# Kernel tuning notes

Measured on AMD Instinct MI355X. Metric: run time of the kernel, lower is better.

## Reference

```python
import jax, jax.numpy as jnp
import numpy as np
from jax import lax

BS, K, N = 8, 8, 16            # batch, gathers per sample, picks per curve
T, WG = 3072, 64               # gather time samples, traces
H, WC = 256, 256               # CVEncoder ScaleSize
RH, RW = 1024, 512             # resize (also GatherEncoder outLen=RH)
T0, T1 = 0.0, 7000.0           # tInt[0], tInt[-1]


def setup_inputs() -> dict:
    key = jax.random.key(0)
    ks = jax.random.split(key, 8)
    gather = jax.random.normal(ks[0], (BS, K, T, WG), jnp.float32)
    # cv: times sorted, strictly > 0, within [T0, T1]; velocities within VMM range
    times = jnp.sort(jax.random.uniform(ks[1], (BS, K, N), minval=100.0, maxval=T1), axis=-1)
    vels = jnp.sort(jax.random.uniform(ks[2], (BS, K, N), minval=1500.0, maxval=4500.0), axis=-1)
    cv = jnp.stack([times, vels], axis=-1).astype(jnp.float32)
    VMM = jnp.tile(jnp.array([1500.0, 4500.0], jnp.float32), (BS, 1))
    def cw(k, shape):
        return (jax.random.normal(k, shape, jnp.float32) * 0.1)
    params = dict(
        w1=cw(ks[3], (1, 1, 3, 3)), b1=jnp.zeros((1,), jnp.float32), g1=jnp.ones((1,), jnp.float32), be1=jnp.zeros((1,), jnp.float32),
        w2=cw(ks[4], (2, 3, 3, 3)), b2=jnp.zeros((2,), jnp.float32), g2=jnp.ones((2,), jnp.float32), be2=jnp.zeros((2,), jnp.float32),
        w3=cw(ks[5], (1, 2, 3, 2)), b3=jnp.zeros((1,), jnp.float32), g3=jnp.ones((1,), jnp.float32), be3=jnp.zeros((1,), jnp.float32),
        wf=cw(ks[6], (1, 1, 3, 3)), bf=jnp.zeros((1,), jnp.float32), gf=jnp.ones((1,), jnp.float32), bef=jnp.zeros((1,), jnp.float32),
    )
    return {"gather": gather, "cv": cv, "VMM": VMM, **params}


def _conv(x, w, b, stride, pad):
    y = lax.conv_general_dilated(x, w, stride, pad, dimension_numbers=("NCHW", "OIHW", "NCHW"))
    return y + b[None, :, None, None]


def _bn(x, g, b, eps=1e-5):
    # training-mode BatchNorm2d: stats over (N, H, W)
    m = jnp.mean(x, (0, 2, 3), keepdims=True)
    v = jnp.var(x, (0, 2, 3), keepdims=True)
    return (x - m) / jnp.sqrt(v + eps) * g[None, :, None, None] + b[None, :, None, None]


def _lrelu(x):
    return jnp.where(x >= 0, x, 0.1 * x)


def _cbl(x, w, b, g, be, stride):
    return _lrelu(_bn(_conv(x, w, b, stride, "VALID"), g, be))


def _maxpool(x, k):
    p = k // 2
    return lax.reduce_window(x, -jnp.inf, lax.max, (1, 1, k, k), (1, 1, 1, 1),
                             ((0, 0), (0, 0), (p, p), (p, p)))


def _cv_mask(cv, VMM):
    # normalize times to fractional row index and velocities to fractional col index
    dt = (T1 - T0) / (H - 1)
    t_idx = (cv[..., 0] - T0) / dt                                        # (BS,K,N)
    dv = (VMM[:, 1] - VMM[:, 0]) / (WC - 1)                               # (BS,)
    v_idx = (cv[..., 1] - VMM[:, 0, None, None]) / dv[:, None, None]      # (BS,K,N)
    t_flat = t_idx.reshape(-1, N)
    v_flat = v_idx.reshape(-1, N)
    tq = jnp.arange(H, dtype=jnp.float32)
    # per-curve piecewise-linear interpolation of v over the time grid
    v_curve = jax.vmap(lambda xp, fp: jnp.interp(tq, xp, fp))(t_flat, v_flat)  # (M,H)
    v_int = jnp.clip(v_curve.astype(jnp.int32), 0, WC - 1)
    M = BS * K
    mask = jnp.full((M, H, WC), 0.01, jnp.float32)
    mask = mask.at[jnp.arange(M)[:, None], jnp.arange(H)[None, :], v_int].add(0.9)
    mask = mask.reshape(BS, K, H, WC)
    # bilinear resize, half-pixel centers == torch align_corners=False
    return jax.image.resize(mask, (BS, K, RH, RW), method="linear")


def _forward(gather, cv, VMM, w1, b1, g1, be1, w2, b2, g2, be2, w3, b3, g3, be3, wf, bf, gf, bef):
    cv_mask = lax.stop_gradient(_cv_mask(cv, VMM))          # CVEncoder runs under no_grad
    x = gather.reshape(-1, 1, T, WG)                        # (BS*K,1,T,WG)
    x = x / jnp.max(jnp.abs(x))                             # mode='mute': keep sign
    x = _cbl(x, w1, b1, g1, be1, (3, 2))                    # (M,1,1024,31)
    xcat = jnp.concatenate([x, _maxpool(x, 3), _maxpool(x, 5)], axis=1)
    x = _cbl(xcat, w2, b2, g2, be2, (3, 2))                 # (M,2,341,15)
    x = _cbl(x, w3, b3, g3, be3, (3, 2))                    # (M,1,113,7)
    x = jax.image.resize(x, (x.shape[0], 1, RH, 1), method="linear")
    genr = x.reshape(BS, K, RH, 1)
    mix = jnp.sum(genr * cv_mask, axis=1, keepdims=True)    # (BS,1,RH,RW)
    y = _conv(mix, wf, bf, (1, 1), ((1, 1), (1, 1)))
    return _lrelu(_bn(y, gf, bef))


def reference(gather, cv, VMM, w1, b1, g1, be1, w2, b2, g2, be2, w3, b3, g3, be3, wf, bf, gf, bef):
    return _forward(gather, cv, VMM, w1, b1, g1, be1, w2, b2, g2, be2, w3, b3, g3, be3, wf, bf, gf, bef)
```

## Files before the change

kernel.cpp:

```cpp
#include <hip/hip_runtime.h>
#include <math.h>

#define BSZ 8
#define KG  8
#define NP  16
#define MM  64
#define TT  3072
#define WGN 64
#define HH  256
#define WCN 256
#define RHN 1024
#define RWN 512

#define C1H 1024
#define C1W 31
#define C2H 341
#define C2W 15
#define C3H 113
#define C3W 7

#define N1 (MM*C1H*C1W)
#define N2 (MM*C2H*C2W)
#define N3 (MM*C3H*C3W)
#define NF (BSZ*RHN*RWN)

#define SL 8

#define OFF_VINT 768
#define OFF_Y1   (OFF_VINT + MM*HH*4)
#define OFF_Y2   (OFF_Y1  + N1*4)
#define OFF_Y3   (OFF_Y2  + 2*N2*4)
#define OFF_GENR (OFF_Y3  + N3*4)

__device__ __forceinline__ void blockAdd2(double s, double ss, double* o0, double* o1) {
    __shared__ double red[4][2];
    __syncthreads();
    int lane = threadIdx.x & 63, wid = threadIdx.x >> 6;
#pragma unroll
    for (int off = 32; off > 0; off >>= 1) {
        s  += __shfl_down(s,  off, 64);
        ss += __shfl_down(ss, off, 64);
    }
    if (lane == 0) { red[wid][0] = s; red[wid][1] = ss; }
    __syncthreads();
    if (threadIdx.x == 0) {
        double a = 0, b = 0;
        int nw = blockDim.x >> 6;
        for (int i = 0; i < nw; i++) { a += red[i][0]; b += red[i][1]; }
        int slot = blockIdx.x & (SL - 1);
        atomicAdd(&o0[slot], a); atomicAdd(&o1[slot], b);
    }
}

__device__ __forceinline__ float2 bn_ab(const double* __restrict__ sums, int c,
                                        const float* __restrict__ g,
                                        const float* __restrict__ be, double n) {
    double sum = 0, sumsq = 0;
#pragma unroll
    for (int j = 0; j < SL; j++) {
        sum   += sums[(2 * c) * SL + j];
        sumsq += sums[(2 * c + 1) * SL + j];
    }
    double mean = sum / n;
    double var  = sumsq / n - mean * mean;
    double a = (double)g[c] / sqrt(var + 1e-5);
    return make_float2((float)a, (float)((double)be[c] - mean * a));
}

__global__ void k_conv1(const float* __restrict__ g, const float* __restrict__ w1,
                        const float* __restrict__ b1,
                        float* __restrict__ y1, double* sums) {
    float w[9];
#pragma unroll
    for (int i = 0; i < 9; i++) w[i] = w1[i];
    float bb = b1[0];
    double s = 0, ss = 0;
    int stride = gridDim.x * blockDim.x;
    for (int idx = blockIdx.x * blockDim.x + threadIdx.x; idx < N1; idx += stride) {
        int ow = idx % C1W;
        int t2 = idx / C1W;
        int oh = t2 % C1H;
        int m  = t2 / C1H;
        const float* xp = g + (size_t)m * TT * WGN + (size_t)(oh * 3) * WGN + ow * 2;
        float acc = bb;
#pragma unroll
        for (int r = 0; r < 3; r++)
#pragma unroll
            for (int c = 0; c < 3; c++) acc += w[r * 3 + c] * xp[r * WGN + c];
        y1[idx] = acc;
        s += acc; ss += (double)acc * (double)acc;
    }
    blockAdd2(s, ss, &sums[0], &sums[SL]);
}

#define F2_OH 32
#define F2_NCH 11
#define F2_NRMAX (3*F2_OH + 4)
__global__ void k_fused2(const float* __restrict__ y1, const double* __restrict__ sums_r,
                         const float* __restrict__ g1, const float* __restrict__ be1,
                         const float* __restrict__ w2, const float* __restrict__ b2,
                         float* __restrict__ y2, double* sums) {
    __shared__ float sact[F2_NRMAX][32];
    __shared__ float sr3[F2_NRMAX][32];
    __shared__ float sr5[F2_NRMAX][32];
    float2 ab1 = bn_ab(sums_r, 0, g1, be1, (double)N1);
    int m   = blockIdx.x / F2_NCH;
    int ch  = blockIdx.x % F2_NCH;
    int oh0 = ch * F2_OH;
    int OHa = min(F2_OH, C2H - oh0);
    int NR  = 3 * OHa + 4;
    int gl0 = 3 * oh0 - 2;
    const float* yp = y1 + (size_t)m * C1H * C1W;
    for (int i = threadIdx.x; i < NR * C1W; i += blockDim.x) {
        int l = i / C1W, w = i % C1W;
        int gr = gl0 + l;
        float v = -INFINITY;
        if (gr >= 0 && gr < C1H) {
            v = ab1.x * yp[gr * C1W + w] + ab1.y;
            v = v >= 0.f ? v : 0.1f * v;
        }
        sact[l][w] = v;
    }
    __syncthreads();
    for (int i = threadIdx.x; i < NR * C1W; i += blockDim.x) {
        int l = i / C1W, w = i % C1W;
        int wl1 = max(w - 1, 0), wr1 = min(w + 1, C1W - 1);
        int wl2 = max(w - 2, 0), wr2 = min(w + 2, C1W - 1);
        float c  = sact[l][w];
        float m3 = fmaxf(fmaxf(sact[l][wl1], c), sact[l][wr1]);
        float m5 = fmaxf(fmaxf(m3, sact[l][wl2]), sact[l][wr2]);
        sr3[l][w] = m3;
        sr5[l][w] = m5;
    }
    __syncthreads();
    double s0 = 0, ss0 = 0, s1 = 0, ss1 = 0;
    for (int o = threadIdx.x; o < OHa * C2W; o += blockDim.x) {
        int lo = o / C2W, ow = o % C2W;
        float a0 = b2[0], acc1 = b2[1];
#pragma unroll
        for (int i = 0; i < 3; i++) {
            int l = 3 * lo + 2 + i;
#pragma unroll
            for (int j = 0; j < 3; j++) {
                int wc = 2 * ow + j;
                float v0 = sact[l][wc];
                float v1 = fmaxf(fmaxf(sr3[l - 1][wc], sr3[l][wc]), sr3[l + 1][wc]);
                float v2 = fmaxf(fmaxf(fmaxf(sr5[l - 2][wc], sr5[l - 1][wc]), sr5[l][wc]),
                                 fmaxf(sr5[l + 1][wc], sr5[l + 2][wc]));
                int ki = i * 3 + j;
                a0   += w2[ki] * v0 + w2[9 + ki] * v1 + w2[18 + ki] * v2;
                acc1 += w2[27 + ki] * v0 + w2[36 + ki] * v1 + w2[45 + ki] * v2;
            }
        }
        size_t ob = (size_t)m * (2 * C2H * C2W) + (size_t)(oh0 + lo) * C2W + ow;
        y2[ob] = a0;
        y2[ob + C2H * C2W] = acc1;
        s0 += a0; ss0 += (double)a0 * a0;
        s1 += acc1; ss1 += (double)acc1 * acc1;
    }
    blockAdd2(s0, ss0, &sums[2 * SL], &sums[3 * SL]);
    blockAdd2(s1, ss1, &sums[4 * SL], &sums[5 * SL]);
}

__global__ void k_conv3(const float* __restrict__ y2, const double* __restrict__ sums_r,
                        const float* __restrict__ g2, const float* __restrict__ be2,
                        const float* __restrict__ w3, const float* __restrict__ b3,
                        float* __restrict__ y3, double* sums) {
    float2 ab20 = bn_ab(sums_r + 2 * SL, 0, g2, be2, (double)N2);
    float2 ab21 = bn_ab(sums_r + 2 * SL, 1, g2, be2, (double)N2);
    double s = 0, ss = 0;
    int stride = gridDim.x * blockDim.x;
    for (int idx = blockIdx.x * blockDim.x + threadIdx.x; idx < N3; idx += stride) {
        int ow = idx % C3W;
        int t2 = idx / C3W;
        int oh = t2 % C3H;
        int m  = t2 / C3H;
        float acc = b3[0];
#pragma unroll
        for (int i = 0; i < 2; i++) {
            float aa = i ? ab21.x : ab20.x, bb = i ? ab21.y : ab20.y;
            const float* cp = y2 + (size_t)m * (2 * C2H * C2W) + (size_t)i * C2H * C2W
                              + (size_t)(oh * 3) * C2W + ow * 2;
#pragma unroll
            for (int r = 0; r < 3; r++)
#pragma unroll
                for (int c = 0; c < 2; c++) {
                    float v = aa * cp[r * C2W + c] + bb;
                    v = v >= 0.f ? v : 0.1f * v;
                    acc += w3[i * 6 + r * 2 + c] * v;
                }
        }
        y3[idx] = acc;
        s += acc; ss += (double)acc * acc;
    }
    blockAdd2(s, ss, &sums[6 * SL], &sums[7 * SL]);
}

__global__ void k_vintgenr(const float* __restrict__ cv, const float* __restrict__ VMM,
                           const float* __restrict__ y3, const double* __restrict__ sums_r,
                           const float* __restrict__ g3, const float* __restrict__ be3,
                           int* __restrict__ vint, float* __restrict__ genr) {
    __shared__ float tt[NP], vv[NP];
    __shared__ float tile[C3H * C3W];
    int m = blockIdx.x;
    int b = m >> 3;
    float2 ab3 = bn_ab(sums_r + 6 * SL, 0, g3, be3, (double)N3);
    if (threadIdx.x < NP) {
        int n = threadIdx.x;
        float t = cv[(m * NP + n) * 2 + 0];
        float v = cv[(m * NP + n) * 2 + 1];
        float dt = 7000.0f / 255.0f;
        tt[n] = t / dt;
        float vmin = VMM[b * 2], vmax = VMM[b * 2 + 1];
        float dv = (vmax - vmin) / 255.0f;
        vv[n] = (v - vmin) / dv;
    }
    for (int i = threadIdx.x; i < C3H * C3W; i += blockDim.x) {
        float v = ab3.x * y3[m * C3H * C3W + i] + ab3.y;
        tile[i] = v >= 0.f ? v : 0.1f * v;
    }
    __syncthreads();
    {
        int h = threadIdx.x;
        float x = (float)h;
        float val;
        if (x <= tt[0]) val = vv[0];
        else if (x >= tt[NP - 1]) val = vv[NP - 1];
        else {
            int i = 1;
            while (i < NP - 1 && tt[i] <= x) i++;
            float d = tt[i] - tt[i - 1];
            val = (d != 0.f) ? vv[i - 1] + (x - tt[i - 1]) / d * (vv[i] - vv[i - 1]) : vv[i];
        }
        int vi = (int)val;
        vint[m * HH + h] = max(0, min(WCN - 1, vi));
    }
    const float cw0 = 4.f / 37.f, cw1 = 5.f / 37.f, cw2 = 6.f / 37.f, cw3 = 7.f / 37.f;
    const float cw[7] = { cw0, cw1, cw2, cw3, cw2, cw1, cw0 };
    for (int i = threadIdx.x; i < RHN; i += blockDim.x) {
        float sh = (i + 0.5f) * (113.0f / 1024.0f) - 0.5f;
        float fl = floorf(sh);
        float fr = sh - fl;
        int i0 = (int)fl, i1 = i0 + 1;
        i0 = max(0, min(C3H - 1, i0));
        i1 = max(0, min(C3H - 1, i1));
        float acc = 0.f;
#pragma unroll
        for (int x = 0; x < 7; x++) {
            float v = (1.f - fr) * tile[i0 * C3W + x] + fr * tile[i1 * C3W + x];
            acc += cw[x] * v;
        }
        genr[m * RHN + i] = acc;
    }
}

#define MC_TH 16
__device__ __forceinline__ void build_mix_tile(const float* __restrict__ genr,
                                               const int* __restrict__ vint,
                                               int b, int h0,
                                               float (*tile)[RWN + 2], float* Grow) {
    for (int i = threadIdx.x; i < (MC_TH + 2) * (RWN + 2); i += blockDim.x)
        ((float*)tile)[i] = 0.f;
    if (threadIdx.x < MC_TH + 2) Grow[threadIdx.x] = 0.f;
    __syncthreads();
    if (threadIdx.x < (MC_TH + 2) * KG) {
        int r = threadIdx.x / KG, k = threadIdx.x % KG;
        int h = h0 - 1 + r;
        if (h >= 0 && h < RHN) {
            int m = b * KG + k;
            float g = genr[m * RHN + h];
            atomicAdd(&Grow[r], g);
            float sh = (h + 0.5f) * 0.25f - 0.5f;
            float fl = floorf(sh);
            float fh = sh - fl;
            int ih0 = (int)fl, ih1 = ih0 + 1;
            ih0 = max(0, min(HH - 1, ih0));
            ih1 = max(0, min(HH - 1, ih1));
            int vv[2] = { vint[m * HH + ih0], vint[m * HH + ih1] };
            float aa[2] = { 0.9f * g * (1.f - fh), 0.9f * g * fh };
#pragma unroll
            for (int t = 0; t < 2; t++) {
                int v = vv[t]; float A = aa[t];
                if (v == 0) {
                    atomicAdd(&tile[r][1 + 0], A);
                    atomicAdd(&tile[r][1 + 1], 0.75f * A);
                    atomicAdd(&tile[r][1 + 2], 0.25f * A);
                } else if (v == WCN - 1) {
                    atomicAdd(&tile[r][1 + 509], 0.25f * A);
                    atomicAdd(&tile[r][1 + 510], 0.75f * A);
                    atomicAdd(&tile[r][1 + 511], A);
                } else {
                    atomicAdd(&tile[r][1 + 2 * v - 1], 0.25f * A);
                    atomicAdd(&tile[r][1 + 2 * v],     0.75f * A);
                    atomicAdd(&tile[r][1 + 2 * v + 1], 0.75f * A);
                    atomicAdd(&tile[r][1 + 2 * v + 2], 0.25f * A);
                }
            }
        }
    }
    __syncthreads();
    for (int i = threadIdx.x; i < (MC_TH + 2) * RWN; i += blockDim.x) {
        int r = i / RWN, w = i % RWN;
        int h = h0 - 1 + r;
        if (h >= 0 && h < RHN) tile[r][w + 1] += 0.01f * Grow[r];
    }
    __syncthreads();
}

__global__ void k_mixA(const float* __restrict__ genr, const int* __restrict__ vint,
                       const float* __restrict__ wf, const float* __restrict__ bf,
                       double* sums) {
    __shared__ float tile[MC_TH + 2][RWN + 2];
    __shared__ float Grow[MC_TH + 2];
    int b   = blockIdx.x / (RHN / MC_TH);
    int h0  = (blockIdx.x % (RHN / MC_TH)) * MC_TH;
    build_mix_tile(genr, vint, b, h0, tile, Grow);
    float w[9];
#pragma unroll
    for (int i = 0; i < 9; i++) w[i] = wf[i];
    float bb = bf[0];
    double s = 0, ss = 0;
    for (int o = threadIdx.x; o < MC_TH * RWN; o += blockDim.x) {
        int lr = o / RWN, x = o % RWN;
        float acc = bb;
#pragma unroll
        for (int dr = 0; dr < 3; dr++)
#pragma unroll
            for (int dc = 0; dc < 3; dc++)
                acc += w[dr * 3 + dc] * tile[lr + dr][x + dc];
        s += acc; ss += (double)acc * acc;
    }
    blockAdd2(s, ss, &sums[8 * SL], &sums[9 * SL]);
}

__global__ void k_mixB(const float* __restrict__ genr, const int* __restrict__ vint,
                       const float* __restrict__ wf, const float* __restrict__ bf,
                       const double* __restrict__ sums_r, const float* __restrict__ gf,
                       const float* __restrict__ bef, float* __restrict__ out) {
    __shared__ float tile[MC_TH + 2][RWN + 2];
    __shared__ float Grow[MC_TH + 2];
    float2 abf = bn_ab(sums_r + 8 * SL, 0, gf, bef, (double)NF);
    int b   = blockIdx.x / (RHN / MC_TH);
    int h0  = (blockIdx.x % (RHN / MC_TH)) * MC_TH;
    build_mix_tile(genr, vint, b, h0, tile, Grow);
    float w[9];
#pragma unroll
    for (int i = 0; i < 9; i++) w[i] = wf[i];
    float bb = bf[0];
    for (int o = threadIdx.x; o < MC_TH * RWN; o += blockDim.x) {
        int lr = o / RWN, x = o % RWN;
        float acc = bb;
#pragma unroll
        for (int dr = 0; dr < 3; dr++)
#pragma unroll
            for (int dc = 0; dc < 3; dc++)
                acc += w[dr * 3 + dc] * tile[lr + dr][x + dc];
        float v = abf.x * acc + abf.y;
        out[((size_t)b * RHN + (h0 + lr)) * RWN + x] = v >= 0.f ? v : 0.1f * v;
    }
}

extern "C" void kernel_launch(void* const* d_in, const int* in_sizes, int n_in,
                              void* d_out, int out_size, void* d_ws, size_t ws_size,
                              hipStream_t stream) {
    const float* gather = (const float*)d_in[0];
    const float* cv     = (const float*)d_in[1];
    const float* VMM    = (const float*)d_in[2];
    const float* w1 = (const float*)d_in[3];
    const float* b1 = (const float*)d_in[4];
    const float* g1 = (const float*)d_in[5];
    const float* be1 = (const float*)d_in[6];
    const float* w2 = (const float*)d_in[7];
    const float* b2 = (const float*)d_in[8];
    const float* g2 = (const float*)d_in[9];
    const float* be2 = (const float*)d_in[10];
    const float* w3 = (const float*)d_in[11];
    const float* b3 = (const float*)d_in[12];
    const float* g3 = (const float*)d_in[13];
    const float* be3 = (const float*)d_in[14];
    const float* wf = (const float*)d_in[15];
    const float* bf = (const float*)d_in[16];
    const float* gf = (const float*)d_in[17];
    const float* bef = (const float*)d_in[18];
    float* out = (float*)d_out;

    char* ws = (char*)d_ws;
    double* sums = (double*)ws;
    int*   vint  = (int*)(ws + OFF_VINT);
    float* y1    = (float*)(ws + OFF_Y1);
    float* y2    = (float*)(ws + OFF_Y2);
    float* y3    = (float*)(ws + OFF_Y3);
    float* genr  = (float*)(ws + OFF_GENR);

    hipMemsetAsync(d_ws, 0, 640, stream);

    k_conv1<<<512, 256, 0, stream>>>(gather, w1, b1, y1, sums);
    k_fused2<<<MM * F2_NCH, 256, 0, stream>>>(y1, sums, g1, be1, w2, b2, y2, sums);
    k_conv3<<<198, 256, 0, stream>>>(y2, sums, g2, be2, w3, b3, y3, sums);
    k_vintgenr<<<MM, 256, 0, stream>>>(cv, VMM, y3, sums, g3, be3, vint, genr);
    k_mixA<<<BSZ * (RHN / MC_TH), 256, 0, stream>>>(genr, vint, wf, bf, sums);
    k_mixB<<<BSZ * (RHN / MC_TH), 256, 0, stream>>>(genr, vint, wf, bf, sums, gf, bef, out);
}
```

Baseline: 196.9 us.

## Stage conv1 input in LDS, write raw mix conv once, apply BN in separate pass

conv1 now assigns one 32-row output tile per block and stages the 96x64 input slab into shared memory with float4 loads, instead of using a grid-stride loop over global memory. The mix stage no longer rebuilds the scatter tile twice: k_mixA stores the raw conv output, and a new vectorized k_act4 kernel applies the final BN and leaky ReLU in place. The fused2 shared arrays get padded to avoid bank conflicts, and conv3 launches one thread per output. The cost is an extra read and write pass over the 16 MB output in place of a second scatter-and-convolve.

```diff
diff --git a/kernel.cpp b/kernel.cpp
--- a/kernel.cpp
+++ b/kernel.cpp
@@ -45,8 +45,8 @@
     __syncthreads();
     if (threadIdx.x == 0) {
         double a = 0, b = 0;
-        int nw = blockDim.x >> 6;
-        for (int i = 0; i < nw; i++) { a += red[i][0]; b += red[i][1]; }
+#pragma unroll
+        for (int i = 0; i < 4; i++) { a += red[i][0]; b += red[i][1]; }
         int slot = blockIdx.x & (SL - 1);
         atomicAdd(&o0[slot], a); atomicAdd(&o1[slot], b);
     }
@@ -70,25 +70,34 @@
 __global__ void k_conv1(const float* __restrict__ g, const float* __restrict__ w1,
                         const float* __restrict__ b1,
                         float* __restrict__ y1, double* sums) {
+    __shared__ float S[96][WGN];
+    int tile = blockIdx.x;
+    int m = tile >> 5, t32 = tile & 31;
+    int oh0 = t32 * 32;
+    const float4* g4 = (const float4*)(g + (size_t)m * TT * WGN + (size_t)(3 * oh0) * WGN);
+    float4* s4 = (float4*)S;
+#pragma unroll
+    for (int i = threadIdx.x; i < 96 * WGN / 4; i += 256) s4[i] = g4[i];
+    __syncthreads();
     float w[9];
 #pragma unroll
     for (int i = 0; i < 9; i++) w[i] = w1[i];
     float bb = b1[0];
     double s = 0, ss = 0;
-    int stride = gridDim.x * blockDim.x;
-    for (int idx = blockIdx.x * blockDim.x + threadIdx.x; idx < N1; idx += stride) {
-        int ow = idx % C1W;
-        int t2 = idx / C1W;
-        int oh = t2 % C1H;
-        int m  = t2 / C1H;
-        const float* xp = g + (size_t)m * TT * WGN + (size_t)(oh * 3) * WGN + ow * 2;
-        float acc = bb;
-#pragma unroll
-        for (int r = 0; r < 3; r++)
-#pragma unroll
-            for (int c = 0; c < 3; c++) acc += w[r * 3 + c] * xp[r * WGN + c];
-        y1[idx] = acc;
-        s += acc; ss += (double)acc * (double)acc;
+#pragma unroll
+    for (int j = 0; j < 4; j++) {
+        int o = threadIdx.x + j * 256;
+        if (o < 32 * C1W) {
+            int lo = o / C1W, ow = o % C1W;
+            float acc = bb;
+#pragma unroll
+            for (int r = 0; r < 3; r++)
+#pragma unroll
+                for (int c = 0; c < 3; c++)
+                    acc += w[r * 3 + c] * S[3 * lo + r][2 * ow + c];
+            y1[(size_t)m * C1H * C1W + (size_t)(oh0 + lo) * C1W + ow] = acc;
+            s += acc; ss += (double)acc * acc;
+        }
     }
     blockAdd2(s, ss, &sums[0], &sums[SL]);
 }
@@ -96,13 +105,14 @@
 #define F2_OH 32
 #define F2_NCH 11
 #define F2_NRMAX (3*F2_OH + 4)
+#define F2_PW 33
 __global__ void k_fused2(const float* __restrict__ y1, const double* __restrict__ sums_r,
                          const float* __restrict__ g1, const float* __restrict__ be1,
                          const float* __restrict__ w2, const float* __restrict__ b2,
                          float* __restrict__ y2, double* sums) {
-    __shared__ float sact[F2_NRMAX][32];
-    __shared__ float sr3[F2_NRMAX][32];
-    __shared__ float sr5[F2_NRMAX][32];
+    __shared__ float sact[F2_NRMAX][F2_PW];
+    __shared__ float sr3[F2_NRMAX][F2_PW];
+    __shared__ float sr5[F2_NRMAX][F2_PW];
     float2 ab1 = bn_ab(sums_r, 0, g1, be1, (double)N1);
     int m   = blockIdx.x / F2_NCH;
     int ch  = blockIdx.x % F2_NCH;
@@ -169,8 +179,8 @@
     float2 ab20 = bn_ab(sums_r + 2 * SL, 0, g2, be2, (double)N2);
     float2 ab21 = bn_ab(sums_r + 2 * SL, 1, g2, be2, (double)N2);
     double s = 0, ss = 0;
-    int stride = gridDim.x * blockDim.x;
-    for (int idx = blockIdx.x * blockDim.x + threadIdx.x; idx < N3; idx += stride) {
+    int idx = blockIdx.x * blockDim.x + threadIdx.x;
+    if (idx < N3) {
         int ow = idx % C3W;
         int t2 = idx / C3W;
         int oh = t2 % C3H;
@@ -235,8 +245,8 @@
         int vi = (int)val;
         vint[m * HH + h] = max(0, min(WCN - 1, vi));
     }
-    const float cw0 = 4.f / 37.f, cw1 = 5.f / 37.f, cw2 = 6.f / 37.f, cw3 = 7.f / 37.f;
-    const float cw[7] = { cw0, cw1, cw2, cw3, cw2, cw1, cw0 };
+    const float cwv[7] = { 4.f/37.f, 5.f/37.f, 6.f/37.f, 7.f/37.f,
+                           6.f/37.f, 5.f/37.f, 4.f/37.f };
     for (int i = threadIdx.x; i < RHN; i += blockDim.x) {
         float sh = (i + 0.5f) * (113.0f / 1024.0f) - 0.5f;
         float fl = floorf(sh);
@@ -248,17 +258,20 @@
 #pragma unroll
         for (int x = 0; x < 7; x++) {
             float v = (1.f - fr) * tile[i0 * C3W + x] + fr * tile[i1 * C3W + x];
-            acc += cw[x] * v;
+            acc += cwv[x] * v;
         }
         genr[m * RHN + i] = acc;
     }
 }
 
 #define MC_TH 16
-__device__ __forceinline__ void build_mix_tile(const float* __restrict__ genr,
-                                               const int* __restrict__ vint,
-                                               int b, int h0,
-                                               float (*tile)[RWN + 2], float* Grow) {
+__global__ void k_mixA(const float* __restrict__ genr, const int* __restrict__ vint,
+                       const float* __restrict__ wf, const float* __restrict__ bf,
+                       float* __restrict__ out, double* sums) {
+    __shared__ float tile[MC_TH + 2][RWN + 2];
+    __shared__ float Grow[MC_TH + 2];
+    int b  = blockIdx.x / (RHN / MC_TH);
+    int h0 = (blockIdx.x % (RHN / MC_TH)) * MC_TH;
     for (int i = threadIdx.x; i < (MC_TH + 2) * (RWN + 2); i += blockDim.x)
         ((float*)tile)[i] = 0.f;
     if (threadIdx.x < MC_TH + 2) Grow[threadIdx.x] = 0.f;
@@ -276,11 +289,11 @@
             int ih0 = (int)fl, ih1 = ih0 + 1;
             ih0 = max(0, min(HH - 1, ih0));
             ih1 = max(0, min(HH - 1, ih1));
-            int vv[2] = { vint[m * HH + ih0], vint[m * HH + ih1] };
-            float aa[2] = { 0.9f * g * (1.f - fh), 0.9f * g * fh };
+            int vv2[2] = { vint[m * HH + ih0], vint[m * HH + ih1] };
+            float aa2[2] = { 0.9f * g * (1.f - fh), 0.9f * g * fh };
 #pragma unroll
             for (int t = 0; t < 2; t++) {
-                int v = vv[t]; float A = aa[t];
+                int v = vv2[t]; float A = aa2[t];
                 if (v == 0) {
                     atomicAdd(&tile[r][1 + 0], A);
                     atomicAdd(&tile[r][1 + 1], 0.75f * A);
@@ -305,59 +318,38 @@
         if (h >= 0 && h < RHN) tile[r][w + 1] += 0.01f * Grow[r];
     }
     __syncthreads();
-}
-
-__global__ void k_mixA(const float* __restrict__ genr, const int* __restrict__ vint,
-                       const float* __restrict__ wf, const float* __restrict__ bf,
-                       double* sums) {
-    __shared__ float tile[MC_TH + 2][RWN + 2];
-    __shared__ float Grow[MC_TH + 2];
-    int b   = blockIdx.x / (RHN / MC_TH);
-    int h0  = (blockIdx.x % (RHN / MC_TH)) * MC_TH;
-    build_mix_tile(genr, vint, b, h0, tile, Grow);
     float w[9];
 #pragma unroll
     for (int i = 0; i < 9; i++) w[i] = wf[i];
     float bb = bf[0];
     double s = 0, ss = 0;
-    for (int o = threadIdx.x; o < MC_TH * RWN; o += blockDim.x) {
-        int lr = o / RWN, x = o % RWN;
+#pragma unroll
+    for (int j = 0; j < 32; j++) {
+        int o  = threadIdx.x + j * 256;
+        int lr = o >> 9, x = o & 511;
         float acc = bb;
 #pragma unroll
         for (int dr = 0; dr < 3; dr++)
 #pragma unroll
             for (int dc = 0; dc < 3; dc++)
                 acc += w[dr * 3 + dc] * tile[lr + dr][x + dc];
+        out[((size_t)b * RHN + (h0 + lr)) * RWN + x] = acc;
         s += acc; ss += (double)acc * acc;
     }
     blockAdd2(s, ss, &sums[8 * SL], &sums[9 * SL]);
 }
 
-__global__ void k_mixB(const float* __restrict__ genr, const int* __restrict__ vint,
-                       const float* __restrict__ wf, const float* __restrict__ bf,
-                       const double* __restrict__ sums_r, const float* __restrict__ gf,
-                       const float* __restrict__ bef, float* __restrict__ out) {
-    __shared__ float tile[MC_TH + 2][RWN + 2];
-    __shared__ float Grow[MC_TH + 2];
+__global__ void k_act4(float4* __restrict__ x, const double* __restrict__ sums_r,
+                       const float* __restrict__ gf, const float* __restrict__ bef) {
     float2 abf = bn_ab(sums_r + 8 * SL, 0, gf, bef, (double)NF);
-    int b   = blockIdx.x / (RHN / MC_TH);
-    int h0  = (blockIdx.x % (RHN / MC_TH)) * MC_TH;
-    build_mix_tile(genr, vint, b, h0, tile, Grow);
-    float w[9];
-#pragma unroll
-    for (int i = 0; i < 9; i++) w[i] = wf[i];
-    float bb = bf[0];
-    for (int o = threadIdx.x; o < MC_TH * RWN; o += blockDim.x) {
-        int lr = o / RWN, x = o % RWN;
-        float acc = bb;
-#pragma unroll
-        for (int dr = 0; dr < 3; dr++)
-#pragma unroll
-            for (int dc = 0; dc < 3; dc++)
-                acc += w[dr * 3 + dc] * tile[lr + dr][x + dc];
-        float v = abf.x * acc + abf.y;
-        out[((size_t)b * RHN + (h0 + lr)) * RWN + x] = v >= 0.f ? v : 0.1f * v;
-    }
+    int i = blockIdx.x * blockDim.x + threadIdx.x;
+    float a = abf.x, b = abf.y;
+    float4 v = x[i];
+    v.x = a * v.x + b; v.x = v.x >= 0.f ? v.x : 0.1f * v.x;
+    v.y = a * v.y + b; v.y = v.y >= 0.f ? v.y : 0.1f * v.y;
+    v.z = a * v.z + b; v.z = v.z >= 0.f ? v.z : 0.1f * v.z;
+    v.w = a * v.w + b; v.w = v.w >= 0.f ? v.w : 0.1f * v.w;
+    x[i] = v;
 }
 
 extern "C" void kernel_launch(void* const* d_in, const int* in_sizes, int n_in,
@@ -394,10 +386,10 @@
 
     hipMemsetAsync(d_ws, 0, 640, stream);
 
-    k_conv1<<<512, 256, 0, stream>>>(gather, w1, b1, y1, sums);
+    k_conv1<<<MM * 32, 256, 0, stream>>>(gather, w1, b1, y1, sums);
     k_fused2<<<MM * F2_NCH, 256, 0, stream>>>(y1, sums, g1, be1, w2, b2, y2, sums);
-    k_conv3<<<198, 256, 0, stream>>>(y2, sums, g2, be2, w3, b3, y3, sums);
+    k_conv3<<<(N3 + 255) / 256, 256, 0, stream>>>(y2, sums, g2, be2, w3, b3, y3, sums);
     k_vintgenr<<<MM, 256, 0, stream>>>(cv, VMM, y3, sums, g3, be3, vint, genr);
-    k_mixA<<<BSZ * (RHN / MC_TH), 256, 0, stream>>>(genr, vint, wf, bf, sums);
-    k_mixB<<<BSZ * (RHN / MC_TH), 256, 0, stream>>>(genr, vint, wf, bf, sums, gf, bef, out);
-}
+    k_mixA<<<BSZ * (RHN / MC_TH), 256, 0, stream>>>(genr, vint, wf, bf, out, sums);
+    k_act4<<<NF / 4 / 256, 256, 0, stream>>>((float4*)out, sums, gf, bef);
+}
```

New measurement: 202.8 us. 1.03x slower.
